# Kernel optimization log

Measured on AMD Instinct MI355X. Metric: run time of the kernel, lower is better.

## Reference

```python
import jax, jax.numpy as jnp
import numpy as np

# Config matching init_kwargs: input_shape=(512,512,28), stride=2
M, N, L = 512, 512, 28
STRIDE = 2
B = 8


def setup_inputs() -> dict:
    key = jax.random.key(0)
    kx, kp = jax.random.split(key)
    x = jax.random.normal(kx, (B, L, M, N), dtype=jnp.float32)
    # phi = (1 + sign(randn)) / 2  -> binary {0,1} mask of shape (M, N)
    phi = (jax.random.normal(kp, (M, N)) > 0).astype(jnp.float32)
    return {"x": x, "phi": phi}


def reference(x, phi):
    """CASSI forward: get_transpose(get_measurement(x, phi), phi, mask_mul=True).

    x:   (b, L, M, N) hyperspectral cube
    phi: (M, N) coded aperture, broadcast across L bands
    """
    b, l, m, n = x.shape
    n_out = n + STRIDE * (l - 1)

    # --- get_measurement: mask-multiply then per-band shift-and-accumulate ---
    y1 = x * phi[None, None, :, :]                      # (b, L, M, N)
    # column index each (band, col) lands in after dispersion shift
    scat_idx = (STRIDE * jnp.arange(l)[:, None] + jnp.arange(n)[None, :]).reshape(-1)  # (L*N,)
    y1f = y1.transpose(0, 2, 1, 3).reshape(b, m, l * n)  # (b, M, L*N)
    y2 = jnp.zeros((b, m, n_out), dtype=x.dtype).at[:, :, scat_idx].add(y1f)  # (b, M, Nout)
    # y_norm=False: no normalization

    # --- get_transpose: gather shifted windows (width = y.shape[-2] = M) ---
    gat_idx = STRIDE * jnp.arange(l)[:, None] + jnp.arange(m)[None, :]  # (L, M)
    xt = y2[:, :, gat_idx]             # (b, M, L, M)
    xt = jnp.moveaxis(xt, 2, 1)        # (b, L, M, M)
    return xt * phi[None, None, :, :]  # mask_mul=True
```

## Files before the change

### kernel.cpp

```cpp
#include <hip/hip_runtime.h>


#define M_DIM 512
#define N_DIM 512
#define L_DIM 28
#define B_DIM 8
#define MN_DIM (M_DIM * N_DIM)
#define NOUT (N_DIM + 2 * (L_DIM - 1))

typedef float v2f __attribute__((ext_vector_type(2)));

__global__ __launch_bounds__(256) void cassi_fwd_kernel(
    const float* __restrict__ x, const float* __restrict__ phi,
    float* __restrict__ out)
{
    __shared__ float sphi[N_DIM];
    __shared__ float sy2[NOUT + 2];

    const int tid = threadIdx.x;
    const int bm  = blockIdx.x;
    const int b   = bm >> 9;
    const int m   = bm & (M_DIM - 1);

    {
        const v2f* phi2 = (const v2f*)(phi + (size_t)m * N_DIM);
        ((v2f*)sphi)[tid] = phi2[tid];
    }
    __syncthreads();

    const v2f p2 = ((const v2f*)sphi)[tid];

    const float* xrow0 = x + (size_t)b * L_DIM * MN_DIM + (size_t)m * N_DIM;

    v2f xv[L_DIM];
#pragma unroll
    for (int l = 0; l < L_DIM; ++l) {
        const int n = (tid >= l) ? 2 * (tid - l) : (N_DIM - 2 * l + 2 * tid);
        xv[l] = *(const v2f*)(xrow0 + (size_t)l * MN_DIM + n);
    }

    v2f acc0 = {0.f, 0.f};
    v2f acc1 = {0.f, 0.f};
#pragma unroll
    for (int l = 0; l < L_DIM; ++l) {
        const int n = (tid >= l) ? 2 * (tid - l) : (N_DIM - 2 * l + 2 * tid);
        const v2f pv = *(const v2f*)(sphi + n);
        const v2f prod = xv[l] * pv;
        if (tid >= l) acc0 += prod;
        else          acc1 += prod;
    }
    *(v2f*)(sy2 + 2 * tid) = acc0;
    if (tid < L_DIM - 1) {
        *(v2f*)(sy2 + N_DIM + 2 * tid) = acc1;
    }
    __syncthreads();

    float* orow0 = out + (size_t)b * L_DIM * MN_DIM + (size_t)m * N_DIM;
#pragma unroll
    for (int l = 0; l < L_DIM; ++l) {
        const v2f y = *(const v2f*)(sy2 + 2 * l + 2 * tid);
        const v2f o = p2 * y;
        __builtin_nontemporal_store(o, (v2f*)(orow0 + (size_t)l * MN_DIM + 2 * tid));
    }
}

extern "C" void kernel_launch(void* const* d_in, const int* in_sizes, int n_in,
                              void* d_out, int out_size, void* d_ws, size_t ws_size,
                              hipStream_t stream) {
    const float* x   = (const float*)d_in[0];
    const float* phi = (const float*)d_in[1];
    float* out       = (float*)d_out;
    cassi_fwd_kernel<<<dim3(B_DIM * M_DIM), dim3(256), 0, stream>>>(x, phi, out);
}
```

Before: 394.4 us.

## Process two rows per block with 128-bit loads and stores

Each 256-thread block now handles two image rows, 128 threads per row, and every thread owns four columns. Global loads of x and phi and the output stores are widened from 64-bit to 128-bit. Band pairs are processed together so the odd-band shift lands via cross-lane shuffles, and boundary tail terms are computed separately. The aim is fewer, wider memory transactions in a bandwidth-bound kernel. The cost is more complex indexing, lane-0 fallback loads and a divergent tail path.

```diff
diff --git a/kernel.cpp b/kernel.cpp
--- a/kernel.cpp
+++ b/kernel.cpp
@@ -6,61 +6,101 @@
 #define L_DIM 28
 #define B_DIM 8
 #define MN_DIM (M_DIM * N_DIM)
-#define NOUT (N_DIM + 2 * (L_DIM - 1))
+#define NT 14
+#define U_DIM 14
 
 typedef float v2f __attribute__((ext_vector_type(2)));
+typedef float v4f __attribute__((ext_vector_type(4)));
 
 __global__ __launch_bounds__(256) void cassi_fwd_kernel(
     const float* __restrict__ x, const float* __restrict__ phi,
     float* __restrict__ out)
 {
-    __shared__ float sphi[N_DIM];
-    __shared__ float sy2[NOUT + 2];
+    __shared__ __align__(16) float sphi[2][N_DIM];
+    __shared__ __align__(16) float sy2[2][576];
 
     const int tid = threadIdx.x;
+    const int r   = tid >> 7;
+    const int t   = tid & 127;
     const int bm  = blockIdx.x;
-    const int b   = bm >> 9;
-    const int m   = bm & (M_DIM - 1);
+    const int b   = bm >> 8;
+    const int m   = ((bm & 255) << 1) | r;
 
-    {
-        const v2f* phi2 = (const v2f*)(phi + (size_t)m * N_DIM);
-        ((v2f*)sphi)[tid] = phi2[tid];
-    }
+    const float* xrow = x + (size_t)b * L_DIM * MN_DIM + (size_t)m * N_DIM;
+
+    v4f pq = *(const v4f*)(phi + (size_t)m * N_DIM + 4 * t);
+    *(v4f*)&sphi[r][4 * t] = pq;
     __syncthreads();
 
-    const v2f p2 = ((const v2f*)sphi)[tid];
+    const float* sphif = &sphi[r][0];
+    const bool lane0 = ((tid & 63) == 0);
 
-    const float* xrow0 = x + (size_t)b * L_DIM * MN_DIM + (size_t)m * N_DIM;
+    v4f acc  = {0.f, 0.f, 0.f, 0.f};
+    v4f acct = {0.f, 0.f, 0.f, 0.f};
 
-    v2f xv[L_DIM];
+#pragma unroll
+    for (int u = 0; u < U_DIM; ++u) {
+        const int s  = t - u;
+        const int sc = s < 0 ? 0 : s;
+        const float* re = xrow + (size_t)(2 * u) * MN_DIM;
+        const float* ro = xrow + (size_t)(2 * u + 1) * MN_DIM;
+        v4f xe = *(const v4f*)(re + 4 * sc);
+        v4f xo = *(const v4f*)(ro + 4 * sc);
+        v4f P  = *(const v4f*)(sphif + 4 * sc);
+        v4f ze = xe * P;
+        v4f zo = xo * P;
+
+        if (s >= 0) acc += ze;
+
+        float lo0 = __shfl_up(zo.z, 1, 64);
+        float lo1 = __shfl_up(zo.w, 1, 64);
+        if (lane0 && s >= 1) {
+            v2f xl = *(const v2f*)(ro + 4 * s - 2);
+            v2f pl = *(const v2f*)(sphif + 4 * s - 2);
+            lo0 = xl.x * pl.x;
+            lo1 = xl.y * pl.y;
+        }
+        if (s >= 1) { acc.x += lo0;  acc.y += lo1; }
+        if (s >= 0) { acc.z += zo.x; acc.w += zo.y; }
+
+        if (t < NT) {
+            if (u == t) {
+                v2f xl = *(const v2f*)(ro + 510);
+                v2f pl = *(const v2f*)(sphif + 510);
+                acct.x += xl.x * pl.x;
+                acct.y += xl.y * pl.y;
+            } else if (u > t) {
+                const int n0 = 512 + 4 * t - 4 * u;
+                v4f xte = *(const v4f*)(re + n0);
+                v4f Pt  = *(const v4f*)(sphif + n0);
+                acct += xte * Pt;
+                v2f xa = *(const v2f*)(ro + n0 - 2);
+                v2f pa = *(const v2f*)(sphif + n0 - 2);
+                v2f xb = *(const v2f*)(ro + n0);
+                acct.x += xa.x * pa.x;
+                acct.y += xa.y * pa.y;
+                acct.z += xb.x * Pt.x;
+                acct.w += xb.y * Pt.y;
+            }
+        }
+    }
+
+    *(v4f*)&sy2[r][4 * t] = acc;
+    if (t < NT) *(v4f*)&sy2[r][512 + 4 * t] = acct;
+    __syncthreads();
+
+    float* orow = out + (size_t)b * L_DIM * MN_DIM + (size_t)m * N_DIM;
+    const float* sy = &sy2[r][0];
 #pragma unroll
     for (int l = 0; l < L_DIM; ++l) {
-        const int n = (tid >= l) ? 2 * (tid - l) : (N_DIM - 2 * l + 2 * tid);
-        xv[l] = *(const v2f*)(xrow0 + (size_t)l * MN_DIM + n);
-    }
-
-    v2f acc0 = {0.f, 0.f};
-    v2f acc1 = {0.f, 0.f};
-#pragma unroll
-    for (int l = 0; l < L_DIM; ++l) {
-        const int n = (tid >= l) ? 2 * (tid - l) : (N_DIM - 2 * l + 2 * tid);
-        const v2f pv = *(const v2f*)(sphi + n);
-        const v2f prod = xv[l] * pv;
-        if (tid >= l) acc0 += prod;
-        else          acc1 += prod;
-    }
-    *(v2f*)(sy2 + 2 * tid) = acc0;
-    if (tid < L_DIM - 1) {
-        *(v2f*)(sy2 + N_DIM + 2 * tid) = acc1;
-    }
-    __syncthreads();
-
-    float* orow0 = out + (size_t)b * L_DIM * MN_DIM + (size_t)m * N_DIM;
-#pragma unroll
-    for (int l = 0; l < L_DIM; ++l) {
-        const v2f y = *(const v2f*)(sy2 + 2 * l + 2 * tid);
-        const v2f o = p2 * y;
-        __builtin_nontemporal_store(o, (v2f*)(orow0 + (size_t)l * MN_DIM + 2 * tid));
+        v2f ya = *(const v2f*)(sy + 2 * l + 4 * t);
+        v2f yb = *(const v2f*)(sy + 2 * l + 4 * t + 2);
+        v4f o;
+        o.x = pq.x * ya.x;
+        o.y = pq.y * ya.y;
+        o.z = pq.z * yb.x;
+        o.w = pq.w * yb.y;
+        __builtin_nontemporal_store(o, (v4f*)(orow + (size_t)l * MN_DIM + 4 * t));
     }
 }
 
@@ -70,5 +110,5 @@
     const float* x   = (const float*)d_in[0];
     const float* phi = (const float*)d_in[1];
     float* out       = (float*)d_out;
-    cassi_fwd_kernel<<<dim3(B_DIM * M_DIM), dim3(256), 0, stream>>>(x, phi, out);
+    cassi_fwd_kernel<<<dim3(B_DIM * M_DIM / 2), dim3(256), 0, stream>>>(x, phi, out);
 }
```

After: 389.9 us. No clear change (-1.1%).
